# Optimization experiments

Hardware: AMD Instinct MI355X
Metric: run time of the kernel (lower is better)

## Reference

```python
import jax, jax.numpy as jnp
import numpy as np

N = 4096          # residues (2 chains x 2048)
CHAINS = 2
LMAX = 2
L = (LMAX + 1) ** 2            # 9 spherical coefficients
BBC = 32                       # bb_channels
NBB = 3                        # n_bb_atoms - 1
SPH = BBC + NBB                # 35 sphere channels fed to attention
KNN = 20
LRK = 40
HEADS = 8
HC = 32
VC = HC // 4                   # attn_value_channels = 8
EDGE_F = 32                    # 16 RBF + 16 positional
L_IDX = np.repeat(np.arange(LMAX + 1), 2 * np.arange(LMAX + 1) + 1)  # degree of each of the 9 coeffs


def so3_linear(x, w, b):
    # x: [N,L,Cin]; w: [LMAX+1,Cin,Cout] shared across m within each degree l; bias only on l=0
    out = jnp.einsum('nlc,lcd->nld', x, w[L_IDX])
    return out.at[:, 0, :].add(b)


def _rbf(d):
    mu = jnp.linspace(0.0, 20.0, 16)
    sigma = 20.0 / 16
    return jnp.exp(-(((d[..., None] - mu) / sigma) ** 2))


def _edge_pos_embed(src, dst):
    d = (src - dst).astype(jnp.float32)
    freq = jnp.exp(jnp.arange(0, 16, 2, dtype=jnp.float32) * (-np.log(10000.0) / 16))
    ang = d[:, None] * freq
    return jnp.concatenate([jnp.cos(ang), jnp.sin(ang)], axis=-1)


def setup_inputs():
    key = jax.random.key(0)
    ks = jax.random.split(key, 16)
    n = lambda i, shp, s=1.0: jax.random.normal(ks[i], shp) * s
    return {
        'X_ca': n(0, (N, 3), 10.0),
        'bb_rel': n(1, (N, NBB, 3)),
        'bb_features': n(2, (N, L, BBC)),
        'batch': jnp.repeat(jnp.arange(CHAINS), N // CHAINS),
        'x_mask': jax.random.uniform(ks[3], (N,)) < 0.02,
        'noising_mask': jax.random.uniform(ks[4], (N,)) < 0.5,
        'attn_w1': n(5, (2 * SPH + EDGE_F, HC), 0.05), 'attn_b1': jnp.zeros((HC,)),
        'attn_w2': n(6, (HC, HEADS), 0.05), 'attn_b2': jnp.zeros((HEADS,)),
        'wv': n(7, (LMAX + 1, SPH, HEADS * VC), 0.05), 'bv': jnp.zeros((HEADS * VC,)),
        'wo': n(8, (LMAX + 1, HEADS * VC, BBC), 0.05), 'bo': jnp.zeros((BBC,)),
        'wg': n(9, (BBC, BBC), 0.05), 'bg': jnp.zeros((BBC,)),
        'wf': n(10, (LMAX + 1, BBC, BBC), 0.05), 'bf': jnp.zeros((BBC,)),
        'w_xca': n(11, (LMAX + 1, BBC, 1), 0.05), 'b_xca': jnp.zeros((1,)),
        'w_gate': n(12, (BBC, 1), 0.05), 'b_gate': jnp.zeros((1,)),
        'w_bb': n(13, (LMAX + 1, BBC, NBB), 0.05), 'b_bb': jnp.zeros((NBB,)),
    }


def reference(X_ca, bb_rel, bb_features, batch, x_mask, noising_mask,
              attn_w1, attn_b1, attn_w2, attn_b2, wv, bv, wo, bo, wg, bg, wf, bf,
              w_xca, b_xca, w_gate, b_gate, w_bb, b_bb):
    Nn = X_ca.shape[0]
    BIG = jnp.float32(1e30)
    # ---- graph construction (knn_graph + sample_inv_cubic_edges) ----
    x2 = jnp.sum(X_ca * X_ca, axis=-1)
    D2 = jnp.maximum(x2[:, None] + x2[None, :] - 2.0 * (X_ca @ X_ca.T), 0.0)  # [N,N]
    same = batch[:, None] == batch[None, :]
    eye = jnp.eye(Nn, dtype=bool)
    mask_pair = x_mask[:, None] | x_mask[None, :]
    invalid = (~same) | eye | mask_pair
    knn_idx = jax.lax.top_k(-jnp.where(invalid, BIG, D2), KNN)[1]   # [N,KNN] sources per target
    # long-range: inverse-cubic distance weights, Gumbel top-k sampling, excluding knn picks
    logits = jnp.where(invalid, -BIG, -1.5 * jnp.log(D2 + 1e-6))
    rows = jnp.arange(Nn)[:, None]
    logits = logits.at[rows, knn_idx].set(-BIG)
    gumb = jax.random.gumbel(jax.random.key(1), (Nn, Nn))
    lr_idx = jax.lax.top_k(logits + gumb, LRK)[1]                   # [N,LRK]
    src = jnp.concatenate([knn_idx.reshape(-1), lr_idx.reshape(-1)])
    dst = jnp.concatenate([jnp.repeat(jnp.arange(Nn), KNN), jnp.repeat(jnp.arange(Nn), LRK)])
    # ---- edge features: RBF(dist) + relative positional embedding ----
    dvec = X_ca[src] - X_ca[dst]
    dist = jnp.linalg.norm(dvec, axis=-1)
    edge_feat = jnp.concatenate([_rbf(dist), _edge_pos_embed(src, dst)], axis=-1)  # [M,32]
    # ---- assemble SO3 node embedding [N,L,35] ----
    node = jnp.zeros((Nn, L, SPH), X_ca.dtype)
    node = node.at[:, :, :BBC].set(bb_features)
    node = node.at[:, 1:4, BBC:].set(jnp.swapaxes(bb_rel, -1, -2))  # l=1 coeffs carry bb_rel
    node = node.at[:, 0, SPH - 1].set(noising_mask.astype(X_ca.dtype))
    # ---- equivariant graph attention (simplified TransBlockV2) ----
    inv = node[:, 0, :]                                             # invariant (l=0) features
    a_in = jnp.concatenate([inv[src], inv[dst], edge_feat], axis=-1)
    h = jax.nn.silu(a_in @ attn_w1 + attn_b1)
    logit = h @ attn_w2 + attn_b2                                   # [M,HEADS]
    mx = jax.ops.segment_max(logit, dst, num_segments=Nn)
    p = jnp.exp(logit - mx[dst])
    Z = jax.ops.segment_sum(p, dst, num_segments=Nn)
    alpha = p / (Z[dst] + 1e-9)                                     # segment softmax per target/head
    v = so3_linear(node, wv, bv)[src].reshape(-1, L, HEADS, VC)     # gather source values
    msg = (v * alpha[:, None, :, None]).reshape(-1, L, HEADS * VC)
    agg = jax.ops.segment_sum(msg, dst, num_segments=Nn)            # scatter to targets
    out = so3_linear(agg, wo, bo)                                   # [N,L,32]
    gate = jax.nn.silu(out[:, 0, :] @ wg + bg)                      # invariant-gated FFN
    out = out + so3_linear(out, wf, bf) * gate[:, None, :]
    # ---- coordinate / backbone updates ----
    upd_x = so3_linear(out, w_xca, b_xca)                           # [N,L,1]
    vec = upd_x[:, 1:4, 0]                                          # l=1 -> 3-vector
    g2 = jax.nn.softplus(out[:, 0, :] @ w_gate + b_gate)            # [N,1]
    new_X = X_ca + jnp.where(noising_mask[:, None], vec * g2, 0.0)
    upd_bb = so3_linear(out, w_bb, b_bb)                            # [N,L,3]
    dbb = jnp.swapaxes(upd_bb[:, 1:4, :], -1, -2)                   # [N,3,3]
    new_bb = bb_rel + jnp.where(noising_mask[:, None, None], dbb, 0.0)
    return new_X, new_bb, out
```

## Files before the change

kernel.cpp:

```cpp
#include <hip/hip_runtime.h>
#include <hip/hip_bf16.h>
#include <stdint.h>

#define NN 4096
#define CS 2048
#define KNN 20
#define LRK 40
#define EPN 60
#define NE (NN*EPN)
#define SPHC 35
#define BBCC 32
#define NHEAD 8
#define HVD 64
#define HCD 32
#define LT 9

#define INVAL_D2 0xFFFFFFFEu
#define CONSUMED 0xFFFFFFFFu

__device__ __forceinline__ float gumbel_f(int i, int j) {
  uint32_t c = ((uint32_t)(i & 2047) << 12) | (uint32_t)j;
  const uint32_t ks0 = 0u, ks1 = 1u, ks2 = 0x1BD11BDBu;
  uint32_t x0 = c + ks0;
  uint32_t x1 = (c + 0x800000u) + ks1;
#define TF_R(r) { x0 += x1; x1 = (x1 << (r)) | (x1 >> (32 - (r))); x1 ^= x0; }
  TF_R(13) TF_R(15) TF_R(26) TF_R(6)   x0 += ks1; x1 += ks2 + 1u;
  TF_R(17) TF_R(29) TF_R(16) TF_R(24)  x0 += ks2; x1 += ks0 + 2u;
  TF_R(13) TF_R(15) TF_R(26) TF_R(6)   x0 += ks0; x1 += ks1 + 3u;
  TF_R(17) TF_R(29) TF_R(16) TF_R(24)  x0 += ks1; x1 += ks2 + 4u;
  TF_R(13) TF_R(15) TF_R(26) TF_R(6)   x0 += ks2; x1 += ks0 + 5u;
#undef TF_R
  uint32_t b = (i >= 2048) ? x1 : x0;
  float u = __uint_as_float((b >> 9) | 0x3F800000u) - 1.0f;
  u = u + 1.17549435e-38f;
  return -logf(-logf(u));
}

__global__ void prep_kernel(const float* __restrict__ X,
                            const int* __restrict__ batch,
                            const int* __restrict__ xmask,
                            float4* __restrict__ Xw, uint32_t* __restrict__ bm) {
#pragma clang fp contract(off)
  int n = blockIdx.x * blockDim.x + threadIdx.x;
  if (n >= NN) return;
  float x = X[n*3+0], y = X[n*3+1], z = X[n*3+2];
  float x2 = (x*x + y*y) + z*z;
  Xw[n] = make_float4(x, y, z, x2);
  bm[n] = ((uint32_t)batch[n] << 1) | (xmask[n] ? 1u : 0u);
}

__global__ __launch_bounds__(256) void nodeproj_kernel(const float* __restrict__ bbf,
                                                       const int* __restrict__ nmask,
                                                       const float* __restrict__ w1,
                                                       const float* __restrict__ b1,
                                                       float* __restrict__ Pn,
                                                       float* __restrict__ Pd) {
  int tid = threadIdx.x;
  int t = tid & 31;
  int n = blockIdx.x * 8 + (tid >> 5);
  float bv_ = bbf[(size_t)n * (LT*BBCC) + t];
  float an = 0.f, ad = b1[t];
  #pragma unroll 8
  for (int c = 0; c < BBCC; c++) {
    float bc = __shfl(bv_, (tid & 32) + c, 64);
    an = fmaf(bc, w1[c * HCD + t], an);
    ad = fmaf(bc, w1[(SPHC + c) * HCD + t], ad);
  }
  float nm = nmask[n] ? 1.f : 0.f;
  an = fmaf(nm, w1[34 * HCD + t], an);
  ad = fmaf(nm, w1[69 * HCD + t], ad);
  Pn[n * HCD + t] = an;
  Pd[n * HCD + t] = ad;
}

__device__ __forceinline__ void radix_select(uint32_t* val, uint32_t* hist,
                                             uint32_t* sh, uint32_t* eqpos,
                                             int* sel, int k, int base, int cb, int tid) {
  uint32_t vpart = 0, rk = (uint32_t)k;
  for (int shift = 24; shift >= 0; shift -= 8) {
    hist[tid] = 0;
    __syncthreads();
    #pragma unroll
    for (int q = 0; q < 8; q++) {
      uint32_t key = val[tid + (q << 8)];
      if ((((uint64_t)(key ^ vpart)) >> (shift + 8)) == 0)
        atomicAdd(&hist[(key >> shift) & 255u], 1u);
    }
    __syncthreads();
    if (tid < 64) {
      uint32_t c0 = hist[tid*4+0], c1 = hist[tid*4+1], c2 = hist[tid*4+2], c3 = hist[tid*4+3];
      uint32_t s = c0 + c1 + c2 + c3;
      uint32_t cum = s;
      #pragma unroll
      for (int off = 1; off < 64; off <<= 1) {
        uint32_t o = __shfl_up(cum, off, 64);
        if (tid >= off) cum += o;
      }
      uint32_t cumprev = cum - s;
      if (rk > cumprev && rk <= cum) {
        uint32_t r = rk - cumprev, dsel, sub;
        if (r <= c0)            { dsel = 0; sub = 0; }
        else if (r <= c0+c1)    { dsel = 1; sub = c0; }
        else if (r <= c0+c1+c2) { dsel = 2; sub = c0 + c1; }
        else                    { dsel = 3; sub = c0 + c1 + c2; }
        sh[0] = tid*4u + dsel;
        sh[1] = r - sub;
      }
    }
    __syncthreads();
    vpart |= (sh[0] << shift);
    rk = sh[1];
  }
  const uint32_t vstar = vpart;
  if (tid == 0) { sh[2] = 0; sh[3] = 0; }
  __syncthreads();
  #pragma unroll
  for (int q = 0; q < 8; q++) {
    int pos = tid + (q << 8);
    uint32_t key = val[pos];
    if (key < vstar) {
      uint32_t slot = atomicAdd(&sh[2], 1u);
      sel[base + slot] = cb + pos;
    } else if (key == vstar) {
      uint32_t t2 = atomicAdd(&sh[3], 1u);
      if (t2 < 64) eqpos[t2] = (uint32_t)pos;
    }
  }
  __syncthreads();
  if (tid == 0) {
    int have = (int)sh[2];
    int m = (int)sh[3]; if (m > 64) m = 64;
    for (int a = 1; a < m; a++) {
      uint32_t p = eqpos[a]; int b = a - 1;
      while (b >= 0 && eqpos[b] > p) { eqpos[b+1] = eqpos[b]; b--; }
      eqpos[b+1] = p;
    }
    for (int a = 0; a < m && have < k; a++) sel[base + have++] = cb + (int)eqpos[a];
  }
  __syncthreads();
}

__global__ __launch_bounds__(256) void select_kernel(const float4* __restrict__ Xw,
                                                     const uint32_t* __restrict__ bm,
                                                     int* __restrict__ srcO) {
#pragma clang fp contract(off)
  __shared__ uint32_t val[CS];
  __shared__ uint32_t hist[256];
  __shared__ uint32_t sh[4];
  __shared__ uint32_t eqpos[64];
  __shared__ int sel[EPN];
  const int i = blockIdx.x, tid = threadIdx.x;
  const uint32_t bmi = bm[i];

  if (bmi & 1u) {
    if (tid < KNN) srcO[(size_t)i * EPN + tid] = tid;
    else if (tid < EPN) srcO[(size_t)i * EPN + tid] = tid - KNN;
    return;
  }
  const int cb = (int)(bmi >> 1) * CS;
  const float4 xi = Xw[i];

  #pragma unroll
  for (int q = 0; q < 8; q++) {
    int pos = tid + (q << 8);
    int j = cb + pos;
    float4 xj = Xw[j];
    uint32_t bmj = bm[j];
    bool inval = ((bmj & 1u) != 0u) || (j == i);
    float dot = xi.x*xj.x + xi.y*xj.y + xi.z*xj.z;
    float d2r = (xi.w + xj.w) - 2.0f*dot;
    float d2 = d2r > 0.0f ? d2r : 0.0f;
    val[pos] = inval ? INVAL_D2 : __float_as_uint(d2);
  }
  __syncthreads();

  radix_select(val, hist, sh, eqpos, sel, KNN, 0, cb, tid);

  if (tid < KNN) val[sel[tid] - cb] = CONSUMED;
  __syncthreads();

  #pragma unroll
  for (int q = 0; q < 8; q++) {
    int pos = tid + (q << 8);
    uint32_t v = val[pos];
    uint32_t skey;
    if (v >= INVAL_D2) skey = CONSUMED;
    else {
      float d2 = __uint_as_float(v);
      float sc = -1.5f * logf(d2 + 1e-6f) + gumbel_f(i, cb + pos);
      uint32_t u = __float_as_uint(sc);
      uint32_t fl = (u & 0x80000000u) ? ~u : (u | 0x80000000u);
      skey = ~fl;
    }
    val[pos] = skey;
  }
  __syncthreads();

  radix_select(val, hist, sh, eqpos, sel, LRK, KNN, cb, tid);

  if (tid < EPN) srcO[(size_t)i * EPN + tid] = sel[tid];
}

__global__ __launch_bounds__(256) void vmat_kernel(const float* __restrict__ bbf,
                                                   const float* __restrict__ bbrel,
                                                   const int* __restrict__ nmask,
                                                   const float* __restrict__ wv,
                                                   const float* __restrict__ bv,
                                                   float* __restrict__ V) {
  int row = blockIdx.x * 4 + (threadIdx.x >> 6);
  int d = threadIdx.x & 63;
  if (row >= NN * LT) return;
  int n = row / LT, l = row % LT;
  int li = (l == 0) ? 0 : (l < 4 ? 1 : 2);
  const float* w = wv + (size_t)li * SPHC * HVD;
  float acc = (l == 0) ? bv[d] : 0.f;
  const float* nb = bbf + (size_t)(n*LT + l) * BBCC;
  for (int c = 0; c < BBCC; c++) acc = fmaf(nb[c], w[c*HVD + d], acc);
  if (l >= 1 && l < 4) {
    for (int b = 0; b < 3; b++)
      acc = fmaf(bbrel[(size_t)(n*3 + b)*3 + (l-1)], w[(32+b)*HVD + d], acc);
  }
  if (l == 0) acc = fmaf(nmask[n] ? 1.f : 0.f, w[34*HVD + d], acc);
  V[(size_t)row * HVD + d] = acc;
}

__global__ __launch_bounds__(256) void edge_kernel(const int* __restrict__ src,
                                                   const float4* __restrict__ Xw,
                                                   const float* __restrict__ Pn,
                                                   const float* __restrict__ Pd,
                                                   const float* __restrict__ w1,
                                                   const float* __restrict__ w2,
                                                   const float* __restrict__ b2,
                                                   float* __restrict__ logitO) {
  __shared__ float w1cf[BBCC][HCD];
  __shared__ float w2f[HCD][NHEAD];
  __shared__ float b2f[NHEAD];
  __shared__ float ef[8][BBCC];
  __shared__ float hbuf[8][HCD];
  int tid = threadIdx.x;
  for (int q = tid; q < BBCC*HCD; q += 256) w1cf[q >> 5][q & 31] = w1[70*HCD + q];
  if (tid < HCD*NHEAD) w2f[tid >> 3][tid & 7] = w2[tid];
  if (tid < NHEAD) b2f[tid] = b2[tid];
  int sub = tid >> 5, t = tid & 31;
  int e = blockIdx.x * 8 + sub;
  int d = e / EPN;
  int s = src[e];
  float4 xs = Xw[s], xd = Xw[d];
  float dx = xs.x - xd.x, dy = xs.y - xd.y, dz = xs.z - xd.z;
  float dist = sqrtf(dx*dx + dy*dy + dz*dz);
  if (t < 16) {
    float mu = (20.0f / 15.0f) * (float)t;
    float zz = (dist - mu) / 1.25f;
    ef[sub][t] = expf(-zz * zz);
  } else {
    int k = t - 16;
    float del = (float)(s - d);
    float fr = expf((float)(2 * (k & 7)) * -0.5756462732485115f);
    float a = del * fr;
    ef[sub][t] = (k < 8) ? cosf(a) : sinf(a);
  }
  __syncthreads();
  float a = Pn[s * HCD + t] + Pd[d * HCD + t];
  #pragma unroll
  for (int k = 0; k < BBCC; k++) a = fmaf(ef[sub][k], w1cf[k][t], a);
  hbuf[sub][t] = a / (1.f + expf(-a));
  __syncthreads();
  if (tid < 64) {
    int e2 = tid >> 3, hh = tid & 7;
    float lg = b2f[hh];
    #pragma unroll
    for (int c = 0; c < HCD; c++) lg = fmaf(hbuf[e2][c], w2f[c][hh], lg);
    logitO[(size_t)(blockIdx.x * 8 + e2) * NHEAD + hh] = lg;
  }
}

__global__ __launch_bounds__(64) void node_kernel(const int* __restrict__ src,
                                                  const float* __restrict__ logit,
                                                  const float* __restrict__ V,
                                                  const float* __restrict__ wo,
                                                  const float* __restrict__ bo,
                                                  const float* __restrict__ wg,
                                                  const float* __restrict__ bg,
                                                  const float* __restrict__ wf,
                                                  const float* __restrict__ bfb,
                                                  const float* __restrict__ w_xca,
                                                  const float* __restrict__ w_gate,
                                                  const float* __restrict__ b_gate,
                                                  const float* __restrict__ w_bb,
                                                  const float* __restrict__ X,
                                                  const float* __restrict__ bbrel,
                                                  const int* __restrict__ nmask,
                                                  float* __restrict__ out) {
  const int n = blockIdx.x, t = threadIdx.x;
  __shared__ float alpha[EPN][NHEAD];
  __shared__ int slist[EPN];
  __shared__ float agg[LT][HVD];
  __shared__ float o0[LT][BBCC];
  __shared__ float ofin[LT][BBCC];
  __shared__ float gate[BBCC];
  if (t < EPN) slist[t] = src[(size_t)n * EPN + t];
  for (int q = t; q < EPN * NHEAD; q += 64) alpha[q / NHEAD][q % NHEAD] = logit[(size_t)n * 480 + q];
  __syncthreads();
  if (t < NHEAD) {
    float m = -1e30f;
    for (int e = 0; e < EPN; e++) m = fmaxf(m, alpha[e][t]);
    float Z = 0.f;
    for (int e = 0; e < EPN; e++) { float p = expf(alpha[e][t] - m); alpha[e][t] = p; Z += p; }
    float iz = 1.f / (Z + 1e-9f);
    for (int e = 0; e < EPN; e++) alpha[e][t] *= iz;
  }
  __syncthreads();
  {
    const int h = t >> 3;
    float acc[LT];
    #pragma unroll
    for (int l = 0; l < LT; l++) acc[l] = 0.f;
    for (int e = 0; e < EPN; e++) {
      const float* Vp = V + (size_t)slist[e] * (LT * HVD) + t;
      float a = alpha[e][h];
      #pragma unroll
      for (int l = 0; l < LT; l++) acc[l] = fmaf(a, Vp[l * HVD], acc[l]);
    }
    #pragma unroll
    for (int l = 0; l < LT; l++) agg[l][t] = acc[l];
  }
  __syncthreads();
  for (int idx = t; idx < LT * BBCC; idx += 64) {
    int l = idx >> 5, d = idx & 31;
    int li = (l == 0) ? 0 : (l < 4 ? 1 : 2);
    float a = (l == 0) ? bo[d] : 0.f;
    const float* w = wo + (size_t)li * HVD * BBCC;
    for (int c = 0; c < HVD; c++) a = fmaf(agg[l][c], w[c * BBCC + d], a);
    o0[l][d] = a;
  }
  __syncthreads();
  if (t < BBCC) {
    float a = bg[t];
    for (int c = 0; c < BBCC; c++) a = fmaf(o0[0][c], wg[c * BBCC + t], a);
    gate[t] = a / (1.f + expf(-a));
  }
  __syncthreads();
  for (int idx = t; idx < LT * BBCC; idx += 64) {
    int l = idx >> 5, d = idx & 31;
    int li = (l == 0) ? 0 : (l < 4 ? 1 : 2);
    float a = (l == 0) ? bfb[d] : 0.f;
    const float* w = wf + (size_t)li * BBCC * BBCC;
    for (int c = 0; c < BBCC; c++) a = fmaf(o0[l][c], w[c * BBCC + d], a);
    float r = o0[l][d] + a * gate[d];
    ofin[l][d] = r;
    out[49152 + (size_t)n * 288 + idx] = r;
  }
  __syncthreads();
  float a2 = b_gate[0];
  for (int c = 0; c < BBCC; c++) a2 = fmaf(ofin[0][c], w_gate[c], a2);
  float g2 = fmaxf(a2, 0.f) + log1pf(expf(-fabsf(a2)));
  bool noise = nmask[n] != 0;
  if (t < 3) {
    float a = 0.f;
    for (int d2 = 0; d2 < BBCC; d2++) a = fmaf(ofin[1 + t][d2], w_xca[32 + d2], a);
    float nx = X[n * 3 + t] + (noise ? a * g2 : 0.f);
    out[(size_t)n * 3 + t] = nx;
  }
  if (t < 9) {
    int b = t / 3, c = t % 3;
    float a = 0.f;
    for (int d2 = 0; d2 < BBCC; d2++) a = fmaf(ofin[1 + c][d2], w_bb[(32 + d2) * 3 + b], a);
    float nb = bbrel[(size_t)(n * 3 + b) * 3 + c] + (noise ? a : 0.f);
    out[12288 + (size_t)n * 9 + b * 3 + c] = nb;
  }
}

extern "C" void kernel_launch(void* const* d_in, const int* in_sizes, int n_in,
                              void* d_out, int out_size, void* d_ws, size_t ws_size,
                              hipStream_t stream) {
  (void)in_sizes; (void)n_in; (void)out_size;
  const float* X      = (const float*)d_in[0];
  const float* bbrel  = (const float*)d_in[1];
  const float* bbf    = (const float*)d_in[2];
  const int* batch    = (const int*)d_in[3];
  const int* xmask    = (const int*)d_in[4];
  const int* nmask    = (const int*)d_in[5];
  const float* w1     = (const float*)d_in[6];
  const float* b1     = (const float*)d_in[7];
  const float* w2     = (const float*)d_in[8];
  const float* b2     = (const float*)d_in[9];
  const float* wv     = (const float*)d_in[10];
  const float* bv     = (const float*)d_in[11];
  const float* wo     = (const float*)d_in[12];
  const float* bo     = (const float*)d_in[13];
  const float* wg     = (const float*)d_in[14];
  const float* bg     = (const float*)d_in[15];
  const float* wf     = (const float*)d_in[16];
  const float* bfb    = (const float*)d_in[17];
  const float* w_xca  = (const float*)d_in[18];
  const float* w_gate = (const float*)d_in[20];
  const float* b_gate = (const float*)d_in[21];
  const float* w_bb   = (const float*)d_in[22];

  if (ws_size < 18939904) return;
  char* ws = (char*)d_ws;
  uint32_t* bmp   = (uint32_t*)(ws + 0);
  int*      srcl  = (int*)(ws + 16384);
  float*    logit = (float*)(ws + 999424);
  float*    V     = (float*)(ws + 8863744);
  float*    Pn    = (float*)(ws + 8863744);
  float*    Pd    = (float*)(ws + 9388032);
  float4*   Xw    = (float4*)(ws + 9912320);
  float*    out   = (float*)d_out;

  prep_kernel<<<NN / 256, 256, 0, stream>>>(X, batch, xmask, Xw, bmp);
  nodeproj_kernel<<<NN / 8, 256, 0, stream>>>(bbf, nmask, w1, b1, Pn, Pd);
  select_kernel<<<NN, 256, 0, stream>>>(Xw, bmp, srcl);
  edge_kernel<<<NE / 8, 256, 0, stream>>>(srcl, Xw, Pn, Pd, w1, w2, b2, logit);
  vmat_kernel<<<(NN * LT) / 4, 256, 0, stream>>>(bbf, bbrel, nmask, wv, bv, V);
  node_kernel<<<NN, 64, 0, stream>>>(srcl, logit, V, wo, bo, wg, bg, wf, bfb,
                                     w_xca, w_gate, b_gate, w_bb, X, bbrel, nmask, out);
}
```

Measured before the change: 305.1 us.

## Replace 4-pass radix select with 2-level histogram select and simplify Gumbel keys

Top-k selection now does one 2048-bin histogram pass on the top 11 bits, gathers the candidates in the chosen bin, and ranks them exactly by (key, position), replacing four 8-bit radix passes and their barriers. The Gumbel-max score -1.5*log(d2)+G is replaced by the monotone-equivalent key d2^1.5 * (-log u), which drops one log per element and the float sign flip. This cuts synchronisation and transcendental work in the select kernel. The risks are candidate overflow beyond 384 entries in one bin, an O(m^2) ranking loop run by a single wavefront, and slight ordering differences from float rounding in the rewritten key.

Result: faster. 277.4 us (-9.1%).

```diff
diff --git a/kernel.cpp b/kernel.cpp
--- a/kernel.cpp
+++ b/kernel.cpp
@@ -14,11 +14,12 @@
 #define HVD 64
 #define HCD 32
 #define LT 9
+#define MAXC 384
 
 #define INVAL_D2 0xFFFFFFFEu
 #define CONSUMED 0xFFFFFFFFu
 
-__device__ __forceinline__ float gumbel_f(int i, int j) {
+__device__ __forceinline__ float neglogu_f(int i, int j) {
   uint32_t c = ((uint32_t)(i & 2047) << 12) | (uint32_t)j;
   const uint32_t ks0 = 0u, ks1 = 1u, ks2 = 0x1BD11BDBu;
   uint32_t x0 = c + ks0;
@@ -33,7 +34,7 @@
   uint32_t b = (i >= 2048) ? x1 : x0;
   float u = __uint_as_float((b >> 9) | 0x3F800000u) - 1.0f;
   u = u + 1.17549435e-38f;
-  return -logf(-logf(u));
+  return -logf(u);
 }
 
 __global__ void prep_kernel(const float* __restrict__ X,
@@ -73,69 +74,82 @@
   Pd[n * HCD + t] = ad;
 }
 
-__device__ __forceinline__ void radix_select(uint32_t* val, uint32_t* hist,
-                                             uint32_t* sh, uint32_t* eqpos,
-                                             int* sel, int k, int base, int cb, int tid) {
-  uint32_t vpart = 0, rk = (uint32_t)k;
-  for (int shift = 24; shift >= 0; shift -= 8) {
-    hist[tid] = 0;
-    __syncthreads();
+__device__ __forceinline__ void sel2l(uint32_t* val, uint32_t* hist2,
+                                      uint32_t* candk, uint32_t* candp,
+                                      uint32_t* sh, int* sel,
+                                      int k, int base, int cb, int tid) {
+  {
+    uint4* h4 = (uint4*)hist2;
+    uint4 z; z.x = 0; z.y = 0; z.z = 0; z.w = 0;
+    h4[tid] = z; h4[tid + 256] = z;
+  }
+  if (tid == 0) { sh[2] = 0; sh[3] = 0; }
+  __syncthreads();
+  #pragma unroll
+  for (int q = 0; q < 8; q++) {
+    uint32_t key = val[tid + (q << 8)];
+    atomicAdd(&hist2[key >> 21], 1u);
+  }
+  __syncthreads();
+  uint32_t h[8], s = 0;
+  #pragma unroll
+  for (int q = 0; q < 8; q++) { h[q] = hist2[tid*8 + q]; s += h[q]; }
+  uint32_t cum = s;
+  #pragma unroll
+  for (int off = 1; off < 64; off <<= 1) {
+    uint32_t o = __shfl_up(cum, off, 64);
+    if ((tid & 63) >= off) cum += o;
+  }
+  if ((tid & 63) == 63) sh[8 + (tid >> 6)] = cum;
+  __syncthreads();
+  uint32_t woff = 0;
+  for (int w = 0; w < (tid >> 6); w++) woff += sh[8 + w];
+  uint32_t cumAll = cum + woff;
+  uint32_t cumBefore = cumAll - s;
+  uint32_t rk = (uint32_t)k;
+  if (rk > cumBefore && rk <= cumAll) {
+    uint32_t rloc = rk - cumBefore, lp = 0;
+    bool done = false;
     #pragma unroll
     for (int q = 0; q < 8; q++) {
-      uint32_t key = val[tid + (q << 8)];
-      if ((((uint64_t)(key ^ vpart)) >> (shift + 8)) == 0)
-        atomicAdd(&hist[(key >> shift) & 255u], 1u);
-    }
-    __syncthreads();
-    if (tid < 64) {
-      uint32_t c0 = hist[tid*4+0], c1 = hist[tid*4+1], c2 = hist[tid*4+2], c3 = hist[tid*4+3];
-      uint32_t s = c0 + c1 + c2 + c3;
-      uint32_t cum = s;
-      #pragma unroll
-      for (int off = 1; off < 64; off <<= 1) {
-        uint32_t o = __shfl_up(cum, off, 64);
-        if (tid >= off) cum += o;
-      }
-      uint32_t cumprev = cum - s;
-      if (rk > cumprev && rk <= cum) {
-        uint32_t r = rk - cumprev, dsel, sub;
-        if (r <= c0)            { dsel = 0; sub = 0; }
-        else if (r <= c0+c1)    { dsel = 1; sub = c0; }
-        else if (r <= c0+c1+c2) { dsel = 2; sub = c0 + c1; }
-        else                    { dsel = 3; sub = c0 + c1 + c2; }
-        sh[0] = tid*4u + dsel;
-        sh[1] = r - sub;
-      }
-    }
-    __syncthreads();
-    vpart |= (sh[0] << shift);
-    rk = sh[1];
-  }
-  const uint32_t vstar = vpart;
-  if (tid == 0) { sh[2] = 0; sh[3] = 0; }
-  __syncthreads();
+      lp += h[q];
+      if (!done && rloc <= lp) { sh[0] = (uint32_t)(tid*8 + q); sh[1] = rloc - (lp - h[q]); done = true; }
+    }
+  }
+  __syncthreads();
+  const uint32_t B = sh[0], r = sh[1];
   #pragma unroll
   for (int q = 0; q < 8; q++) {
     int pos = tid + (q << 8);
     uint32_t key = val[pos];
-    if (key < vstar) {
-      uint32_t slot = atomicAdd(&sh[2], 1u);
-      sel[base + slot] = cb + pos;
-    } else if (key == vstar) {
-      uint32_t t2 = atomicAdd(&sh[3], 1u);
-      if (t2 < 64) eqpos[t2] = (uint32_t)pos;
-    }
-  }
-  __syncthreads();
-  if (tid == 0) {
-    int have = (int)sh[2];
-    int m = (int)sh[3]; if (m > 64) m = 64;
-    for (int a = 1; a < m; a++) {
-      uint32_t p = eqpos[a]; int b = a - 1;
-      while (b >= 0 && eqpos[b] > p) { eqpos[b+1] = eqpos[b]; b--; }
-      eqpos[b+1] = p;
-    }
-    for (int a = 0; a < m && have < k; a++) sel[base + have++] = cb + (int)eqpos[a];
+    if ((key >> 21) == B) {
+      uint32_t idx = atomicAdd(&sh[2], 1u);
+      if (idx < MAXC) { candk[idx] = key; candp[idx] = (uint32_t)pos; }
+    }
+  }
+  __syncthreads();
+  int m = (int)sh[2]; if (m > MAXC) m = MAXC;
+  if (tid < 64) {
+    for (int ci = tid; ci < m; ci += 64) {
+      unsigned long long k64 = ((unsigned long long)candk[ci] << 32) | candp[ci];
+      uint32_t rank = 0;
+      for (int j = 0; j < m; j++) {
+        unsigned long long o = ((unsigned long long)candk[j] << 32) | candp[j];
+        rank += (o < k64) ? 1u : 0u;
+      }
+      if (rank == r - 1) { sh[0] = candk[ci]; sh[1] = candp[ci]; }
+    }
+  }
+  __syncthreads();
+  const uint32_t vstar = sh[0], istar = sh[1];
+  #pragma unroll
+  for (int q = 0; q < 8; q++) {
+    int pos = tid + (q << 8);
+    uint32_t key = val[pos];
+    if (key < vstar || (key == vstar && (uint32_t)pos <= istar)) {
+      uint32_t slot = atomicAdd(&sh[3], 1u);
+      sel[base + (int)slot] = cb + pos;
+    }
   }
   __syncthreads();
 }
@@ -145,9 +159,10 @@
                                                      int* __restrict__ srcO) {
 #pragma clang fp contract(off)
   __shared__ uint32_t val[CS];
-  __shared__ uint32_t hist[256];
-  __shared__ uint32_t sh[4];
-  __shared__ uint32_t eqpos[64];
+  __shared__ uint32_t hist2[2048];
+  __shared__ uint32_t candk[MAXC];
+  __shared__ uint32_t candp[MAXC];
+  __shared__ uint32_t sh[12];
   __shared__ int sel[EPN];
   const int i = blockIdx.x, tid = threadIdx.x;
   const uint32_t bmi = bm[i];
@@ -174,7 +189,7 @@
   }
   __syncthreads();
 
-  radix_select(val, hist, sh, eqpos, sel, KNN, 0, cb, tid);
+  sel2l(val, hist2, candk, candp, sh, sel, KNN, 0, cb, tid);
 
   if (tid < KNN) val[sel[tid] - cb] = CONSUMED;
   __syncthreads();
@@ -186,17 +201,15 @@
     uint32_t skey;
     if (v >= INVAL_D2) skey = CONSUMED;
     else {
-      float d2 = __uint_as_float(v);
-      float sc = -1.5f * logf(d2 + 1e-6f) + gumbel_f(i, cb + pos);
-      uint32_t u = __float_as_uint(sc);
-      uint32_t fl = (u & 0x80000000u) ? ~u : (u | 0x80000000u);
-      skey = ~fl;
+      float d2p = __uint_as_float(v) + 1e-6f;
+      float w = d2p * sqrtf(d2p) * neglogu_f(i, cb + pos);
+      skey = __float_as_uint(w);
     }
     val[pos] = skey;
   }
   __syncthreads();
 
-  radix_select(val, hist, sh, eqpos, sel, LRK, KNN, cb, tid);
+  sel2l(val, hist2, candk, candp, sh, sel, LRK, KNN, cb, tid);
 
   if (tid < EPN) srcO[(size_t)i * EPN + tid] = sel[tid];
 }
```
